# Optimization experiments

Measured on AMD Instinct MI355X. Metric: run time of the kernel, lower is better.

The kernel has to match this reference:

```python
import jax, jax.numpy as jnp
import numpy as np

NUM_HEADS = 16

def _split_heads(x, H):
    B, S, D = x.shape
    return x.reshape(B, S, H, D // H).transpose(0, 2, 1, 3)  # [B,H,S,hd]

def _merge_heads(x):
    B, H, S, hd = x.shape
    return x.transpose(0, 2, 1, 3).reshape(B, S, H * hd)

def setup_inputs() -> dict:
    key = jax.random.key(0)
    k1, k2, k3, k4 = jax.random.split(key, 4)
    B, S, D = 2, 2048, 1024
    return {
        "visual_features": jax.random.normal(k1, (B, S, D), dtype=jnp.float32),
        "transaction_features": jax.random.normal(k2, (B, S, D), dtype=jnp.float32),
        "W_qkv": jax.random.normal(k3, (D, 3 * D), dtype=jnp.float32) * (1.0 / np.sqrt(D)),
        "W_out": jax.random.normal(k4, (D, D), dtype=jnp.float32) * (1.0 / np.sqrt(D)),
    }

def reference(visual_features, transaction_features, W_qkv, W_out):
    H = NUM_HEADS
    D = visual_features.shape[-1]
    scale = (D // H) ** -0.5

    v_q, v_k, v_v = [_split_heads(t, H) for t in jnp.split(visual_features @ W_qkv, 3, axis=-1)]
    t_q, t_k, t_v = [_split_heads(t, H) for t in jnp.split(transaction_features @ W_qkv, 3, axis=-1)]

    # visual queries attend to transaction keys/values (dropout = identity at eval)
    v2t = jax.nn.softmax(jnp.einsum('bhqd,bhkd->bhqk', v_q, t_k) * scale, axis=-1)
    t2v = jax.nn.softmax(jnp.einsum('bhqd,bhkd->bhqk', t_q, v_k) * scale, axis=-1)

    v2t_out = _merge_heads(jnp.einsum('bhqk,bhkd->bhqd', v2t, t_v))
    t2v_out = _merge_heads(jnp.einsum('bhqk,bhkd->bhqd', t2v, v_v))

    return (v2t_out + t2v_out) @ W_out
```

## Files before the change

kernel.cpp:

```cpp
#include <hip/hip_runtime.h>


typedef short  frag8 __attribute__((ext_vector_type(8)));
typedef float  f32x4 __attribute__((ext_vector_type(4)));

union F8 { frag8 f; uint2 u2[2]; unsigned u[4]; };

#define MFMA16(a,b,c) __builtin_amdgcn_mfma_f32_16x16x32_bf16((a),(b),(c),0,0,0)

__device__ __forceinline__ unsigned short f2bf(float f) {
  unsigned u = __builtin_bit_cast(unsigned, f);
  return (unsigned short)((u + 0x7fffu + ((u >> 16) & 1u)) >> 16);
}
__device__ __forceinline__ float bf2f(unsigned short s) {
  unsigned u = ((unsigned)s) << 16;
  return __builtin_bit_cast(float, u);
}
__device__ __forceinline__ unsigned pkbf(float lo, float hi) {
  unsigned r;
  asm("v_cvt_pk_bf16_f32 %0, %1, %2" : "=v"(r) : "v"(lo), "v"(hi));
  return r;
}
__device__ __forceinline__ float fexp2(float x) {
  float r;
  asm("v_exp_f32 %0, %1" : "=v"(r) : "v"(x));
  return r;
}

__global__ __launch_bounds__(256) void k_pre(
    const float* __restrict__ vis, const float* __restrict__ trn,
    const float* __restrict__ Wqkv, const float* __restrict__ Wout,
    unsigned short* __restrict__ Abf, unsigned short* __restrict__ WqbT,
    unsigned short* __restrict__ WobT)
{
  __shared__ unsigned short L[64 * 72];
  const int bid = blockIdx.x;
  const int tid = threadIdx.x;

  if (bid < 4096) {
    size_t i8 = ((size_t)bid * 256 + tid) * 8;
    const float* src = (i8 < 4194304) ? vis + i8 : trn + (i8 - 4194304);
    float4 u = *(const float4*)src;
    float4 v = *(const float4*)(src + 4);
    uint4 w;
    w.x = pkbf(u.x, u.y); w.y = pkbf(u.z, u.w);
    w.z = pkbf(v.x, v.y); w.w = pkbf(v.z, v.w);
    *(uint4*)(Abf + i8) = w;
    return;
  }

  const float* W; unsigned short* Wt; int N, bx, by;
  if (bid < 4864) { int b = bid - 4096; W = Wqkv; Wt = WqbT; N = 3072; bx = b % 48; by = b / 48; }
  else            { int b = bid - 4864; W = Wout; Wt = WobT; N = 1024; bx = b % 16; by = b / 16; }
  const int n0 = bx * 64, k0 = by * 64;
  {
    int kr = tid >> 2, c4 = (tid & 3) * 16;
    const float* gp = W + (size_t)(k0 + kr) * N + n0 + c4;
    float4 u0 = *(const float4*)gp,       u1 = *(const float4*)(gp + 4);
    float4 u2 = *(const float4*)(gp + 8), u3 = *(const float4*)(gp + 12);
    unsigned* lw = (unsigned*)&L[kr * 72 + c4];
    lw[0] = pkbf(u0.x, u0.y); lw[1] = pkbf(u0.z, u0.w);
    lw[2] = pkbf(u1.x, u1.y); lw[3] = pkbf(u1.z, u1.w);
    lw[4] = pkbf(u2.x, u2.y); lw[5] = pkbf(u2.z, u2.w);
    lw[6] = pkbf(u3.x, u3.y); lw[7] = pkbf(u3.z, u3.w);
  }
  __syncthreads();
  int nr = tid >> 2, kc = (tid & 3) * 16;
  unsigned wb[8];
#pragma unroll
  for (int j = 0; j < 8; ++j) {
    unsigned lo = L[(kc + 2 * j)     * 72 + nr];
    unsigned hi = L[(kc + 2 * j + 1) * 72 + nr];
    wb[j] = lo | (hi << 16);
  }
  unsigned short* op = Wt + (size_t)(n0 + nr) * 1024 + k0 + kc;
  *(uint4*)op       = *(uint4*)&wb[0];
  *(uint4*)(op + 8) = *(uint4*)&wb[4];
}

__global__ __launch_bounds__(256) void k_gemm_qkv_b(
    const unsigned short* __restrict__ Abf, const unsigned short* __restrict__ WqbT,
    unsigned short* __restrict__ qkv)
{
  __shared__ unsigned short As_[128 * 32];
  __shared__ unsigned short Bs_[128 * 32];
  const int tid  = threadIdx.x;
  const int lane = tid & 63, wv = tid >> 6;
  const int lm = lane & 15, lg = lane >> 4;
  const int wg = (blockIdx.x & 7) * 192 + (blockIdx.x >> 3);
  const int nt = wg % 24, mt = wg / 24;
  const int wr = (wv >> 1) * 64, wc = (wv & 1) * 64;

  f32x4 acc[4][4] = {};

  const unsigned short* agp =
      Abf + (size_t)(mt * 128 + wv * 32 + (lane >> 2)) * 1024 + (lane & 3) * 8;
  const unsigned short* bgp =
      WqbT + (size_t)(nt * 128 + wv * 32 + (lane >> 2)) * 1024 + (lane & 3) * 8;

  for (int kt = 0; kt < 32; ++kt) {
    __syncthreads();
    __builtin_amdgcn_global_load_lds(
        (const __attribute__((address_space(1))) void*)(agp + kt * 32),
        (__attribute__((address_space(3))) void*)&As_[wv * 1024], 16, 0, 0);
    __builtin_amdgcn_global_load_lds(
        (const __attribute__((address_space(1))) void*)(agp + 16 * 1024 + kt * 32),
        (__attribute__((address_space(3))) void*)&As_[wv * 1024 + 512], 16, 0, 0);
    __builtin_amdgcn_global_load_lds(
        (const __attribute__((address_space(1))) void*)(bgp + kt * 32),
        (__attribute__((address_space(3))) void*)&Bs_[wv * 1024], 16, 0, 0);
    __builtin_amdgcn_global_load_lds(
        (const __attribute__((address_space(1))) void*)(bgp + 16 * 1024 + kt * 32),
        (__attribute__((address_space(3))) void*)&Bs_[wv * 1024 + 512], 16, 0, 0);
    __syncthreads();
    frag8 af[4], bfr[4];
#pragma unroll
    for (int mi = 0; mi < 4; ++mi)
      af[mi] = *(const frag8*)&As_[(wr + mi * 16 + lm) * 32 + lg * 8];
#pragma unroll
    for (int ni = 0; ni < 4; ++ni)
      bfr[ni] = *(const frag8*)&Bs_[(wc + ni * 16 + lm) * 32 + lg * 8];
#pragma unroll
    for (int mi = 0; mi < 4; ++mi)
#pragma unroll
      for (int ni = 0; ni < 4; ++ni)
        acc[mi][ni] = MFMA16(af[mi], bfr[ni], acc[mi][ni]);
  }

#pragma unroll
  for (int mi = 0; mi < 4; ++mi)
#pragma unroll
    for (int ni = 0; ni < 4; ++ni)
#pragma unroll
      for (int r = 0; r < 4; ++r) {
        int row = mt * 128 + wr + mi * 16 + lg * 4 + r;
        int col = nt * 128 + wc + ni * 16 + lm;
        qkv[(size_t)row * 3072 + col] = f2bf(acc[mi][ni][r]);
      }
}

__global__ __launch_bounds__(256) void k_vt(
    const unsigned short* __restrict__ qkv, unsigned short* __restrict__ Vt)
{
  __shared__ unsigned short L[64 * 72];
  const int tid = threadIdx.x;
  const int sblk = blockIdx.x;
  const int by = blockIdx.y;
  const int src = by >> 4, h = by & 15;
  {
    int sl = tid >> 2, dc = tid & 3;
    const unsigned short* gp =
        qkv + (size_t)(src * 2048 + sblk * 64 + sl) * 3072 + 2048 + h * 64 + dc * 16;
    *(frag8*)&L[sl * 72 + dc * 16]     = *(const frag8*)gp;
    *(frag8*)&L[sl * 72 + dc * 16 + 8] = *(const frag8*)(gp + 8);
  }
  __syncthreads();
  int d = tid >> 2, sc = tid & 3;
  unsigned wbuf[8];
#pragma unroll
  for (int j = 0; j < 8; ++j) {
    unsigned lo = L[(sc * 16 + 2 * j)     * 72 + d];
    unsigned hi = L[(sc * 16 + 2 * j + 1) * 72 + d];
    wbuf[j] = lo | (hi << 16);
  }
  unsigned short* op =
      Vt + ((size_t)(src * 16 + h) * 64 + d) * 2048 + sblk * 64 + sc * 16;
  *(uint4*)op       = *(uint4*)&wbuf[0];
  *(uint4*)(op + 8) = *(uint4*)&wbuf[4];
}

__global__ __launch_bounds__(256) void k_attn(
    const unsigned short* __restrict__ qkv, const unsigned short* __restrict__ Vt,
    unsigned short* __restrict__ o0, unsigned short* __restrict__ o1)
{
  __shared__ unsigned short Ks[4][32 * 72];
  __shared__ unsigned short Vs[4][8 * 272];
  const int tid  = threadIdx.x;
  const int lane = tid & 63, wv = tid >> 6;
  const int lm = lane & 15, lg = lane >> 4;
  const int qt = blockIdx.x, comb = blockIdx.y;
  const int dir = comb >> 5, bb = (comb >> 4) & 1, h = comb & 15;
  const int qbase  = (dir ? 4096 : 0) + bb * 2048;
  const int kvbase = (dir ? 0 : 4096) + bb * 2048;
  const int qcol = h * 64, kcol = 1024 + h * 64;

  const float QS = 0.125f * 1.44269504f;
  frag8 qf[2][2];
#pragma unroll
  for (int mi = 0; mi < 2; ++mi)
#pragma unroll
    for (int kb = 0; kb < 2; ++kb) {
      frag8 t = *(const frag8*)&qkv[
          (size_t)(qbase + qt * 128 + wv * 32 + mi * 16 + lm) * 3072 +
          qcol + kb * 32 + lg * 8];
#pragma unroll
      for (int j = 0; j < 8; ++j)
        t[j] = (short)f2bf(bf2f((unsigned short)t[j]) * QS);
      qf[mi][kb] = t;
    }

  f32x4 acc[2][4] = {};
  float lr[2] = {0.0f, 0.0f};

  const int skv = tid >> 3, sd = (tid & 7) * 8;
  const int vd = tid >> 2, vc = tid & 3;
  const unsigned short* __restrict__ kpp =
      qkv + (size_t)(kvbase + skv) * 3072 + kcol + sd;
  const unsigned short* __restrict__ vpp =
      Vt + ((size_t)((kvbase >> 11) * 16 + h) * 64 + vd) * 2048 + vc * 8;

  frag8 R0k, R0v, R1k, R1v;

#define LOAD2() do {                                                       \
    R0k = *(const frag8*)kpp;  kpp += 32 * 3072;                           \
    R0v = *(const frag8*)vpp;  vpp += 32;                                  \
    R1k = *(const frag8*)kpp;  kpp += 32 * 3072;                           \
    R1v = *(const frag8*)vpp;  vpp += 32;                                  \
  } while (0)

#define WRITE1(s_, Rk_, Rv_) do {                                          \
    *(frag8*)&Ks[s_][skv * 72 + sd] = Rk_;                                 \
    F8 tv_; tv_.f = Rv_;                                                   \
    *(uint2*)&Vs[s_][(2 * vc) * 272 + vd * 4]     = tv_.u2[0];             \
    *(uint2*)&Vs[s_][(2 * vc + 1) * 272 + vd * 4] = tv_.u2[1];             \
  } while (0)

  LOAD2();
  WRITE1(0, R0k, R0v);
  WRITE1(1, R1k, R1v);
  LOAD2();
  __syncthreads();

  for (int j = 0; j < 32; ++j) {
    const int p = j & 1;
    if (j < 31) {
      WRITE1(2 * (p ^ 1),     R0k, R0v);
      WRITE1(2 * (p ^ 1) + 1, R1k, R1v);
    }
    if (j < 30) LOAD2();

    const int sA = 2 * p, sB = 2 * p + 1;

    frag8 kfA[2][2], kfB[2][2];
#pragma unroll
    for (int t = 0; t < 2; ++t)
#pragma unroll
      for (int kb = 0; kb < 2; ++kb) {
        kfA[t][kb] = *(const frag8*)&Ks[sA][(t * 16 + lm) * 72 + kb * 32 + lg * 8];
        kfB[t][kb] = *(const frag8*)&Ks[sB][(t * 16 + lm) * 72 + kb * 32 + lg * 8];
      }
    f32x4 stA[2][2] = {}, stB[2][2] = {};
#pragma unroll
    for (int mi = 0; mi < 2; ++mi)
#pragma unroll
      for (int t = 0; t < 2; ++t)
#pragma unroll
        for (int kb = 0; kb < 2; ++kb) {
          stA[mi][t] = MFMA16(kfA[t][kb], qf[mi][kb], stA[mi][t]);
          stB[mi][t] = MFMA16(kfB[t][kb], qf[mi][kb], stB[mi][t]);
        }

    frag8 paA[2], paB[2];
#pragma unroll
    for (int mi = 0; mi < 2; ++mi) {
      f32x4 a = stA[mi][0], b = stA[mi][1];
      f32x4 c = stB[mi][0], d = stB[mi][1];
      float p0[8], p1[8];
#pragma unroll
      for (int r = 0; r < 4; ++r) {
        p0[r] = fexp2(a[r]); p0[4 + r] = fexp2(b[r]);
        p1[r] = fexp2(c[r]); p1[4 + r] = fexp2(d[r]);
      }
      lr[mi] += (((p0[0] + p0[1]) + (p0[2] + p0[3])) +
                 ((p0[4] + p0[5]) + (p0[6] + p0[7]))) +
                (((p1[0] + p1[1]) + (p1[2] + p1[3])) +
                 ((p1[4] + p1[5]) + (p1[6] + p1[7])));
      F8 ka, kb2;
      ka.u[0]  = pkbf(p0[0], p0[1]); ka.u[1]  = pkbf(p0[2], p0[3]);
      ka.u[2]  = pkbf(p0[4], p0[5]); ka.u[3]  = pkbf(p0[6], p0[7]);
      kb2.u[0] = pkbf(p1[0], p1[1]); kb2.u[1] = pkbf(p1[2], p1[3]);
      kb2.u[2] = pkbf(p1[4], p1[5]); kb2.u[3] = pkbf(p1[6], p1[7]);
      paA[mi] = ka.f;
      paB[mi] = kb2.f;
    }

    frag8 vbA[4], vbB[4];
#pragma unroll
    for (int di = 0; di < 4; ++di) {
      F8 ta, tb;
      ta.u2[0] = *(const uint2*)&Vs[sA][lg * 272 + (di * 16 + lm) * 4];
      ta.u2[1] = *(const uint2*)&Vs[sA][(4 + lg) * 272 + (di * 16 + lm) * 4];
      tb.u2[0] = *(const uint2*)&Vs[sB][lg * 272 + (di * 16 + lm) * 4];
      tb.u2[1] = *(const uint2*)&Vs[sB][(4 + lg) * 272 + (di * 16 + lm) * 4];
      vbA[di] = ta.f;
      vbB[di] = tb.f;
    }
#pragma unroll
    for (int mi = 0; mi < 2; ++mi)
#pragma unroll
      for (int di = 0; di < 4; ++di) {
        acc[mi][di] = MFMA16(paA[mi], vbA[di], acc[mi][di]);
        acc[mi][di] = MFMA16(paB[mi], vbB[di], acc[mi][di]);
      }

    __syncthreads();
  }

#undef LOAD2
#undef WRITE1

  unsigned short* __restrict__ dst = dir ? o1 : o0;
#pragma unroll
  for (int mi = 0; mi < 2; ++mi) {
    float l = lr[mi];
    l += __shfl_xor(l, 16);
    l += __shfl_xor(l, 32);
    float inv = 1.0f / l;
#pragma unroll
    for (int r = 0; r < 4; ++r) {
      float invr = __shfl(inv, 4 * lg + r);
      int row = bb * 2048 + qt * 128 + wv * 32 + mi * 16 + lg * 4 + r;
#pragma unroll
      for (int di = 0; di < 4; ++di) {
        int col = h * 64 + di * 16 + lm;
        dst[(size_t)row * 1024 + col] = f2bf(acc[mi][di][r] * invr);
      }
    }
  }
}

__global__ __launch_bounds__(256) void k_gemm_out_b(
    const unsigned short* __restrict__ x0, const unsigned short* __restrict__ x1,
    const unsigned short* __restrict__ WobT, float* __restrict__ out)
{
  __shared__ unsigned short As[128 * 40];
  __shared__ unsigned short Bs_[128 * 32];
  const int tid  = threadIdx.x;
  const int lane = tid & 63, wv = tid >> 6;
  const int lm = lane & 15, lg = lane >> 4;
  const int wg = (blockIdx.x & 7) * 32 + (blockIdx.x >> 3);
  const int nt = wg % 8, mt = wg / 8;
  const int wr = (wv >> 1) * 64, wc = (wv & 1) * 64;

  f32x4 acc[4][4] = {};

  const int am = tid >> 1, akq = (tid & 1) * 16;
  const int arow = mt * 128 + am;
  const unsigned short* __restrict__ a0p = x0 + (size_t)arow * 1024;
  const unsigned short* __restrict__ a1p = x1 + (size_t)arow * 1024;
  const unsigned short* bgp =
      WobT + (size_t)(nt * 128 + wv * 32 + (lane >> 2)) * 1024 + (lane & 3) * 8;

  for (int kt = 0; kt < 32; ++kt) {
    __syncthreads();
    __builtin_amdgcn_global_load_lds(
        (const __attribute__((address_space(1))) void*)(bgp + kt * 32),
        (__attribute__((address_space(3))) void*)&Bs_[wv * 1024], 16, 0, 0);
    __builtin_amdgcn_global_load_lds(
        (const __attribute__((address_space(1))) void*)(bgp + 16 * 1024 + kt * 32),
        (__attribute__((address_space(3))) void*)&Bs_[wv * 1024 + 512], 16, 0, 0);
    {
      frag8 u0 = *(const frag8*)(a0p + kt * 32 + akq);
      frag8 u1 = *(const frag8*)(a0p + kt * 32 + akq + 8);
      frag8 w0 = *(const frag8*)(a1p + kt * 32 + akq);
      frag8 w1 = *(const frag8*)(a1p + kt * 32 + akq + 8);
      frag8 p0, p1;
#pragma unroll
      for (int j = 0; j < 8; ++j) {
        p0[j] = (short)f2bf(bf2f((unsigned short)u0[j]) + bf2f((unsigned short)w0[j]));
        p1[j] = (short)f2bf(bf2f((unsigned short)u1[j]) + bf2f((unsigned short)w1[j]));
      }
      *(frag8*)&As[am * 40 + akq]     = p0;
      *(frag8*)&As[am * 40 + akq + 8] = p1;
    }
    __syncthreads();
    frag8 af[4], bfr[4];
#pragma unroll
    for (int mi = 0; mi < 4; ++mi)
      af[mi] = *(const frag8*)&As[(wr + mi * 16 + lm) * 40 + lg * 8];
#pragma unroll
    for (int ni = 0; ni < 4; ++ni)
      bfr[ni] = *(const frag8*)&Bs_[(wc + ni * 16 + lm) * 32 + lg * 8];
#pragma unroll
    for (int mi = 0; mi < 4; ++mi)
#pragma unroll
      for (int ni = 0; ni < 4; ++ni)
        acc[mi][ni] = MFMA16(af[mi], bfr[ni], acc[mi][ni]);
  }

#pragma unroll
  for (int mi = 0; mi < 4; ++mi)
#pragma unroll
    for (int ni = 0; ni < 4; ++ni)
#pragma unroll
      for (int r = 0; r < 4; ++r) {
        int row = mt * 128 + wr + mi * 16 + lg * 4 + r;
        int col = nt * 128 + wc + ni * 16 + lm;
        out[(size_t)row * 1024 + col] = acc[mi][ni][r];
      }
}

extern "C" void kernel_launch(void* const* d_in, const int* in_sizes, int n_in,
                              void* d_out, int out_size, void* d_ws, size_t ws_size,
                              hipStream_t stream)
{
  const float* vis  = (const float*)d_in[0];
  const float* trn  = (const float*)d_in[1];
  const float* Wqkv = (const float*)d_in[2];
  const float* Wout = (const float*)d_in[3];
  float* out = (float*)d_out;

  char* base = (char*)d_ws;
  unsigned short* qkv  = (unsigned short*)base;
  unsigned short* a0   = (unsigned short*)(base + 50331648UL);
  unsigned short* a1   = a0 + 4194304;
  unsigned short* Vt   = (unsigned short*)(base + 67108864UL);
  unsigned short* WobT = (unsigned short*)(base + 83886080UL);
  unsigned short* Abf  = (unsigned short*)(base + 87031808UL);
  unsigned short* WqbT = Abf + 8388608;

  k_pre       <<<5120, 256, 0, stream>>>(vis, trn, Wqkv, Wout, Abf, WqbT, WobT);
  k_gemm_qkv_b<<<1536, 256, 0, stream>>>(Abf, WqbT, qkv);
  k_vt        <<<dim3(32, 64), 256, 0, stream>>>(qkv, Vt);
  k_attn      <<<dim3(16, 64), 256, 0, stream>>>(qkv, Vt, a0, a1);
  k_gemm_out_b<<<256, 256, 0, stream>>>(a0, a1, WobT, out);
}
```

Baseline: 220.7 us.

## Compute V transposed directly via separate GEMM and fold Q scale into weights

Splits the QKV projection into a QK GEMM and a separate GEMM that computes V^T = Wv^T · A^T, writing V already transposed. This removes the k_vt transpose kernel and its extra read and write of V. The softmax scale is also folded into the Q columns of the bf16 weight copy, so the attention kernel no longer rescales Q per tile. Applying the scale before bf16 rounding slightly changes the numerics. The V GEMM writes scattered output and adds one more launch in place of the transpose.

```diff
diff --git a/kernel.cpp b/kernel.cpp
--- a/kernel.cpp
+++ b/kernel.cpp
@@ -53,16 +53,17 @@
   if (bid < 4864) { int b = bid - 4096; W = Wqkv; Wt = WqbT; N = 3072; bx = b % 48; by = b / 48; }
   else            { int b = bid - 4864; W = Wout; Wt = WobT; N = 1024; bx = b % 16; by = b / 16; }
   const int n0 = bx * 64, k0 = by * 64;
+  const float sc = (bid < 4864 && n0 < 1024) ? 0.125f * 1.44269504f : 1.0f;
   {
     int kr = tid >> 2, c4 = (tid & 3) * 16;
     const float* gp = W + (size_t)(k0 + kr) * N + n0 + c4;
     float4 u0 = *(const float4*)gp,       u1 = *(const float4*)(gp + 4);
     float4 u2 = *(const float4*)(gp + 8), u3 = *(const float4*)(gp + 12);
     unsigned* lw = (unsigned*)&L[kr * 72 + c4];
-    lw[0] = pkbf(u0.x, u0.y); lw[1] = pkbf(u0.z, u0.w);
-    lw[2] = pkbf(u1.x, u1.y); lw[3] = pkbf(u1.z, u1.w);
-    lw[4] = pkbf(u2.x, u2.y); lw[5] = pkbf(u2.z, u2.w);
-    lw[6] = pkbf(u3.x, u3.y); lw[7] = pkbf(u3.z, u3.w);
+    lw[0] = pkbf(u0.x * sc, u0.y * sc); lw[1] = pkbf(u0.z * sc, u0.w * sc);
+    lw[2] = pkbf(u1.x * sc, u1.y * sc); lw[3] = pkbf(u1.z * sc, u1.w * sc);
+    lw[4] = pkbf(u2.x * sc, u2.y * sc); lw[5] = pkbf(u2.z * sc, u2.w * sc);
+    lw[6] = pkbf(u3.x * sc, u3.y * sc); lw[7] = pkbf(u3.z * sc, u3.w * sc);
   }
   __syncthreads();
   int nr = tid >> 2, kc = (tid & 3) * 16;
@@ -78,17 +79,17 @@
   *(uint4*)(op + 8) = *(uint4*)&wb[4];
 }
 
-__global__ __launch_bounds__(256) void k_gemm_qkv_b(
+__global__ __launch_bounds__(256) void k_gemm_qk(
     const unsigned short* __restrict__ Abf, const unsigned short* __restrict__ WqbT,
-    unsigned short* __restrict__ qkv)
+    unsigned short* __restrict__ qk)
 {
   __shared__ unsigned short As_[128 * 32];
   __shared__ unsigned short Bs_[128 * 32];
   const int tid  = threadIdx.x;
   const int lane = tid & 63, wv = tid >> 6;
   const int lm = lane & 15, lg = lane >> 4;
-  const int wg = (blockIdx.x & 7) * 192 + (blockIdx.x >> 3);
-  const int nt = wg % 24, mt = wg / 24;
+  const int wg = (blockIdx.x & 7) * 128 + (blockIdx.x >> 3);
+  const int nt = wg % 16, mt = wg / 16;
   const int wr = (wv >> 1) * 64, wc = (wv & 1) * 64;
 
   f32x4 acc[4][4] = {};
@@ -135,42 +136,75 @@
       for (int r = 0; r < 4; ++r) {
         int row = mt * 128 + wr + mi * 16 + lg * 4 + r;
         int col = nt * 128 + wc + ni * 16 + lm;
-        qkv[(size_t)row * 3072 + col] = f2bf(acc[mi][ni][r]);
-      }
-}
-
-__global__ __launch_bounds__(256) void k_vt(
-    const unsigned short* __restrict__ qkv, unsigned short* __restrict__ Vt)
-{
-  __shared__ unsigned short L[64 * 72];
-  const int tid = threadIdx.x;
-  const int sblk = blockIdx.x;
-  const int by = blockIdx.y;
-  const int src = by >> 4, h = by & 15;
-  {
-    int sl = tid >> 2, dc = tid & 3;
-    const unsigned short* gp =
-        qkv + (size_t)(src * 2048 + sblk * 64 + sl) * 3072 + 2048 + h * 64 + dc * 16;
-    *(frag8*)&L[sl * 72 + dc * 16]     = *(const frag8*)gp;
-    *(frag8*)&L[sl * 72 + dc * 16 + 8] = *(const frag8*)(gp + 8);
-  }
-  __syncthreads();
-  int d = tid >> 2, sc = tid & 3;
-  unsigned wbuf[8];
-#pragma unroll
-  for (int j = 0; j < 8; ++j) {
-    unsigned lo = L[(sc * 16 + 2 * j)     * 72 + d];
-    unsigned hi = L[(sc * 16 + 2 * j + 1) * 72 + d];
-    wbuf[j] = lo | (hi << 16);
-  }
-  unsigned short* op =
-      Vt + ((size_t)(src * 16 + h) * 64 + d) * 2048 + sblk * 64 + sc * 16;
-  *(uint4*)op       = *(uint4*)&wbuf[0];
-  *(uint4*)(op + 8) = *(uint4*)&wbuf[4];
+        qk[(size_t)row * 2048 + col] = f2bf(acc[mi][ni][r]);
+      }
+}
+
+__global__ __launch_bounds__(256) void k_gemm_vT(
+    const unsigned short* __restrict__ WvT, const unsigned short* __restrict__ Abf,
+    unsigned short* __restrict__ Vt)
+{
+  __shared__ unsigned short As_[128 * 32];
+  __shared__ unsigned short Bs_[128 * 32];
+  const int tid  = threadIdx.x;
+  const int lane = tid & 63, wv = tid >> 6;
+  const int lm = lane & 15, lg = lane >> 4;
+  const int wg = (blockIdx.x & 7) * 64 + (blockIdx.x >> 3);
+  const int nt = wg % 64, mt = wg / 64;
+  const int wr = (wv >> 1) * 64, wc = (wv & 1) * 64;
+
+  f32x4 acc[4][4] = {};
+
+  const unsigned short* agp =
+      WvT + (size_t)(mt * 128 + wv * 32 + (lane >> 2)) * 1024 + (lane & 3) * 8;
+  const unsigned short* bgp =
+      Abf + (size_t)(nt * 128 + wv * 32 + (lane >> 2)) * 1024 + (lane & 3) * 8;
+
+  for (int kt = 0; kt < 32; ++kt) {
+    __syncthreads();
+    __builtin_amdgcn_global_load_lds(
+        (const __attribute__((address_space(1))) void*)(agp + kt * 32),
+        (__attribute__((address_space(3))) void*)&As_[wv * 1024], 16, 0, 0);
+    __builtin_amdgcn_global_load_lds(
+        (const __attribute__((address_space(1))) void*)(agp + 16 * 1024 + kt * 32),
+        (__attribute__((address_space(3))) void*)&As_[wv * 1024 + 512], 16, 0, 0);
+    __builtin_amdgcn_global_load_lds(
+        (const __attribute__((address_space(1))) void*)(bgp + kt * 32),
+        (__attribute__((address_space(3))) void*)&Bs_[wv * 1024], 16, 0, 0);
+    __builtin_amdgcn_global_load_lds(
+        (const __attribute__((address_space(1))) void*)(bgp + 16 * 1024 + kt * 32),
+        (__attribute__((address_space(3))) void*)&Bs_[wv * 1024 + 512], 16, 0, 0);
+    __syncthreads();
+    frag8 af[4], bfr[4];
+#pragma unroll
+    for (int mi = 0; mi < 4; ++mi)
+      af[mi] = *(const frag8*)&As_[(wr + mi * 16 + lm) * 32 + lg * 8];
+#pragma unroll
+    for (int ni = 0; ni < 4; ++ni)
+      bfr[ni] = *(const frag8*)&Bs_[(wc + ni * 16 + lm) * 32 + lg * 8];
+#pragma unroll
+    for (int mi = 0; mi < 4; ++mi)
+#pragma unroll
+      for (int ni = 0; ni < 4; ++ni)
+        acc[mi][ni] = MFMA16(af[mi], bfr[ni], acc[mi][ni]);
+  }
+
+#pragma unroll
+  for (int mi = 0; mi < 4; ++mi)
+#pragma unroll
+    for (int ni = 0; ni < 4; ++ni)
+#pragma unroll
+      for (int r = 0; r < 4; ++r) {
+        int row = mt * 128 + wr + mi * 16 + lg * 4 + r;
+        int col = nt * 128 + wc + ni * 16 + lm;
+        int src = col >> 11;
+        Vt[((size_t)(src * 1024 + row)) * 2048 + (col & 2047)] =
+            f2bf(acc[mi][ni][r]);
+      }
 }
 
 __global__ __launch_bounds__(256) void k_attn(
-    const unsigned short* __restrict__ qkv, const unsigned short* __restrict__ Vt,
+    const unsigned short* __restrict__ qk, const unsigned short* __restrict__ Vt,
     unsigned short* __restrict__ o0, unsigned short* __restrict__ o1)
 {
   __shared__ unsigned short Ks[4][32 * 72];
@@ -184,20 +218,14 @@
   const int kvbase = (dir ? 0 : 4096) + bb * 2048;
   const int qcol = h * 64, kcol = 1024 + h * 64;
 
-  const float QS = 0.125f * 1.44269504f;
   frag8 qf[2][2];
 #pragma unroll
   for (int mi = 0; mi < 2; ++mi)
 #pragma unroll
-    for (int kb = 0; kb < 2; ++kb) {
-      frag8 t = *(const frag8*)&qkv[
-          (size_t)(qbase + qt * 128 + wv * 32 + mi * 16 + lm) * 3072 +
+    for (int kb = 0; kb < 2; ++kb)
+      qf[mi][kb] = *(const frag8*)&qk[
+          (size_t)(qbase + qt * 128 + wv * 32 + mi * 16 + lm) * 2048 +
           qcol + kb * 32 + lg * 8];
-#pragma unroll
-      for (int j = 0; j < 8; ++j)
-        t[j] = (short)f2bf(bf2f((unsigned short)t[j]) * QS);
-      qf[mi][kb] = t;
-    }
 
   f32x4 acc[2][4] = {};
   float lr[2] = {0.0f, 0.0f};
@@ -205,16 +233,16 @@
   const int skv = tid >> 3, sd = (tid & 7) * 8;
   const int vd = tid >> 2, vc = tid & 3;
   const unsigned short* __restrict__ kpp =
-      qkv + (size_t)(kvbase + skv) * 3072 + kcol + sd;
+      qk + (size_t)(kvbase + skv) * 2048 + kcol + sd;
   const unsigned short* __restrict__ vpp =
-      Vt + ((size_t)((kvbase >> 11) * 16 + h) * 64 + vd) * 2048 + vc * 8;
+      Vt + ((size_t)((kvbase >> 11) * 1024 + h * 64 + vd)) * 2048 + vc * 8;
 
   frag8 R0k, R0v, R1k, R1v;
 
 #define LOAD2() do {                                                       \
-    R0k = *(const frag8*)kpp;  kpp += 32 * 3072;                           \
+    R0k = *(const frag8*)kpp;  kpp += 32 * 2048;                           \
     R0v = *(const frag8*)vpp;  vpp += 32;                                  \
-    R1k = *(const frag8*)kpp;  kpp += 32 * 3072;                           \
+    R1k = *(const frag8*)kpp;  kpp += 32 * 2048;                           \
     R1v = *(const frag8*)vpp;  vpp += 32;                                  \
   } while (0)
 
@@ -411,17 +439,17 @@
   float* out = (float*)d_out;
 
   char* base = (char*)d_ws;
-  unsigned short* qkv  = (unsigned short*)base;
-  unsigned short* a0   = (unsigned short*)(base + 50331648UL);
+  unsigned short* qk   = (unsigned short*)base;
+  unsigned short* a0   = (unsigned short*)(base + 33554432UL);
   unsigned short* a1   = a0 + 4194304;
-  unsigned short* Vt   = (unsigned short*)(base + 67108864UL);
-  unsigned short* WobT = (unsigned short*)(base + 83886080UL);
-  unsigned short* Abf  = (unsigned short*)(base + 87031808UL);
-  unsigned short* WqbT = Abf + 8388608;
-
-  k_pre       <<<5120, 256, 0, stream>>>(vis, trn, Wqkv, Wout, Abf, WqbT, WobT);
-  k_gemm_qkv_b<<<1536, 256, 0, stream>>>(Abf, WqbT, qkv);
-  k_vt        <<<dim3(32, 64), 256, 0, stream>>>(qkv, Vt);
-  k_attn      <<<dim3(16, 64), 256, 0, stream>>>(qkv, Vt, a0, a1);
+  unsigned short* Vt   = (unsigned short*)(base + 50331648UL);
+  unsigned short* WobT = (unsigned short*)(base + 67108864UL);
+  unsigned short* Abf  = (unsigned short*)(base + 69206016UL);
+  unsigned short* WqbT = (unsigned short*)(base + 85983232UL);
+
+  k_pre      <<<5120, 256, 0, stream>>>(vis, trn, Wqkv, Wout, Abf, WqbT, WobT);
+  k_gemm_qk  <<<1024, 256, 0, stream>>>(Abf, WqbT, qk);
+  k_gemm_vT  <<<512, 256, 0, stream>>>(WqbT + (size_t)2048 * 1024, Abf, Vt);
+  k_attn     <<<dim3(16, 64), 256, 0, stream>>>(qk, Vt, a0, a1);
   k_gemm_out_b<<<256, 256, 0, stream>>>(a0, a1, WobT, out);
 }
```

Measured after the change: 225.2 us. 1.02x slower.
